# Kernel tuning notes

Measured on AMD Instinct MI355X. Metric: run time of the kernel, lower is better.

## Reference

```python
import jax, jax.numpy as jnp
import numpy as np

B, T, X_DIM = 8192, 100, 256
Y_DIM = 6
KSIZE = 50


def setup_inputs() -> dict:
    key = jax.random.key(0)
    k1, k2, k3 = jax.random.split(key, 3)
    sequence = jax.random.normal(k1, (B, T, X_DIM), dtype=jnp.float32)
    # per-feature Conv1d(1,1,k=50,bias=False) weights, stacked as depthwise kernel [X_DIM, 1, K]
    conv_w = jax.random.normal(k2, (X_DIM, 1, KSIZE), dtype=jnp.float32) * 0.1
    # Linear(x_dim -> y_dim*50, bias=False), torch layout [out, in]
    fc_w = jax.random.normal(k3, (Y_DIM * 50, X_DIM), dtype=jnp.float32) * 0.05
    return {"sequence": sequence, "conv_w": conv_w, "fc_w": fc_w}


def reference(sequence, conv_w, fc_w):
    # slice time window 30:100 and move features to channel dim: [B, X_DIM, 70]
    x = jnp.transpose(sequence[:, 30:100, :], (0, 2, 1))
    f = x.shape[1]
    # the Python loop of per-feature Conv1d(1,1,k) ops == one depthwise (grouped) conv
    y = jax.lax.conv_general_dilated(
        x, conv_w,
        window_strides=(1,), padding="VALID",
        dimension_numbers=("NCH", "OIH", "NCH"),
        feature_group_count=f,
    )  # [B, X_DIM, 21]
    # ReLU then max over time -> [B, X_DIM] (kernel_num == 1, so concat == this)
    feat = jnp.max(jax.nn.relu(y), axis=2)
    out = feat @ fc_w.T  # [B, Y_DIM*50]
    return out.reshape(-1, 50, Y_DIM)
```

## Files before the change

kernel.cpp:

```cpp
#include <hip/hip_runtime.h>

#define B_TOTAL 8192
#define T_FULL  100
#define XD      256
#define T0      30
#define TW      70
#define KS      50
#define NT      21
#define YOUT    300
#define FC_NB   16


#define DECLG(G) float G##0,G##1,G##2,G##3,G##4,G##5,G##6,G##7,G##8,G##9;

#define VMF(N) asm volatile("s_waitcnt vmcnt(" #N ")" ::: "memory")

#define GLL1(c, s, r) \
  __builtin_amdgcn_global_load_lds( \
      (const __attribute__((address_space(1))) void*)(xp + ((c)*10 + (r)) * XD), \
      (__attribute__((address_space(3))) void*)(ldsr + (s)*640 + (r)*64), 4, 0, 0);

#define GLL(c, s) \
  GLL1(c,s,0) GLL1(c,s,1) GLL1(c,s,2) GLL1(c,s,3) GLL1(c,s,4) \
  GLL1(c,s,5) GLL1(c,s,6) GLL1(c,s,7) GLL1(c,s,8) GLL1(c,s,9)

#define LOADL(G, s) \
  G##0=ldsr[(s)*640+  0+lane]; G##1=ldsr[(s)*640+ 64+lane]; \
  G##2=ldsr[(s)*640+128+lane]; G##3=ldsr[(s)*640+192+lane]; \
  G##4=ldsr[(s)*640+256+lane]; G##5=ldsr[(s)*640+320+lane]; \
  G##6=ldsr[(s)*640+384+lane]; G##7=ldsr[(s)*640+448+lane]; \
  G##8=ldsr[(s)*640+512+lane]; G##9=ldsr[(s)*640+576+lane];

#define LOADWSET(W, K0) \
  W##0=wtp[(K0+0)*XD]; W##1=wtp[(K0+1)*XD]; W##2=wtp[(K0+2)*XD]; W##3=wtp[(K0+3)*XD]; W##4=wtp[(K0+4)*XD]; \
  W##5=wtp[(K0+5)*XD]; W##6=wtp[(K0+6)*XD]; W##7=wtp[(K0+7)*XD]; W##8=wtp[(K0+8)*XD]; W##9=wtp[(K0+9)*XD];

#define ROW(A, W, X0,X1,X2,X3,X4,X5,X6,X7,X8,X9) \
  A=fmaf(X0,W##0,A); A=fmaf(X1,W##1,A); A=fmaf(X2,W##2,A); A=fmaf(X3,W##3,A); A=fmaf(X4,W##4,A); \
  A=fmaf(X5,W##5,A); A=fmaf(X6,W##6,A); A=fmaf(X7,W##7,A); A=fmaf(X8,W##8,A); A=fmaf(X9,W##9,A);

#define KB30(W, y0,y1,y2,y3,y4,y5,y6,y7,y8,y9,y10,y11,y12,y13,y14,y15,y16,y17,y18,y19,y20,y21,y22,y23,y24,y25,y26,y27,y28,y29) \
  ROW(a0 , W, y0 ,y1 ,y2 ,y3 ,y4 ,y5 ,y6 ,y7 ,y8 ,y9 ) \
  ROW(a1 , W, y1 ,y2 ,y3 ,y4 ,y5 ,y6 ,y7 ,y8 ,y9 ,y10) \
  ROW(a2 , W, y2 ,y3 ,y4 ,y5 ,y6 ,y7 ,y8 ,y9 ,y10,y11) \
  ROW(a3 , W, y3 ,y4 ,y5 ,y6 ,y7 ,y8 ,y9 ,y10,y11,y12) \
  ROW(a4 , W, y4 ,y5 ,y6 ,y7 ,y8 ,y9 ,y10,y11,y12,y13) \
  ROW(a5 , W, y5 ,y6 ,y7 ,y8 ,y9 ,y10,y11,y12,y13,y14) \
  ROW(a6 , W, y6 ,y7 ,y8 ,y9 ,y10,y11,y12,y13,y14,y15) \
  ROW(a7 , W, y7 ,y8 ,y9 ,y10,y11,y12,y13,y14,y15,y16) \
  ROW(a8 , W, y8 ,y9 ,y10,y11,y12,y13,y14,y15,y16,y17) \
  ROW(a9 , W, y9 ,y10,y11,y12,y13,y14,y15,y16,y17,y18) \
  ROW(a10, W, y10,y11,y12,y13,y14,y15,y16,y17,y18,y19) \
  ROW(a11, W, y11,y12,y13,y14,y15,y16,y17,y18,y19,y20) \
  ROW(a12, W, y12,y13,y14,y15,y16,y17,y18,y19,y20,y21) \
  ROW(a13, W, y13,y14,y15,y16,y17,y18,y19,y20,y21,y22) \
  ROW(a14, W, y14,y15,y16,y17,y18,y19,y20,y21,y22,y23) \
  ROW(a15, W, y15,y16,y17,y18,y19,y20,y21,y22,y23,y24) \
  ROW(a16, W, y16,y17,y18,y19,y20,y21,y22,y23,y24,y25) \
  ROW(a17, W, y17,y18,y19,y20,y21,y22,y23,y24,y25,y26) \
  ROW(a18, W, y18,y19,y20,y21,y22,y23,y24,y25,y26,y27) \
  ROW(a19, W, y19,y20,y21,y22,y23,y24,y25,y26,y27,y28) \
  ROW(a20, W, y20,y21,y22,y23,y24,y25,y26,y27,y28,y29)

#define KB30X(...) KB30(__VA_ARGS__)

#define GA xa0,xa1,xa2,xa3,xa4,xa5,xa6,xa7,xa8,xa9
#define GB xb0,xb1,xb2,xb3,xb4,xb5,xb6,xb7,xb8,xb9
#define GC xc0,xc1,xc2,xc3,xc4,xc5,xc6,xc7,xc8,xc9
#define GD xd0,xd1,xd2,xd3,xd4,xd5,xd6,xd7,xd8,xd9

__global__ __launch_bounds__(256)
void transpose_w(const float* __restrict__ conv_w, const float* __restrict__ fc_w,
                 float* __restrict__ wt, float* __restrict__ fct) {
    const int i = blockIdx.x * 256 + threadIdx.x;
    if (i < XD * KS) {
        const int f = i / KS;
        const int k = i - f * KS;
        wt[k * XD + f] = conv_w[i];
    }
    if (i < YOUT * XD) {
        const int o = i >> 8;
        const int q = i & 255;
        fct[q * YOUT + o] = fc_w[i];
    }
}

__global__ __launch_bounds__(256, 4)
void conv_kernel(const float* __restrict__ seq, const float* __restrict__ wt,
                 float* __restrict__ feat) {
    __shared__ float lds[4 * 4 * 640];
    const int lane = threadIdx.x & 63;
    const int wv   = threadIdx.x >> 6;
    const int b    = blockIdx.x;
    const float* xp  = seq + ((size_t)b * T_FULL + T0) * XD + threadIdx.x;
    const float* wtp = wt + threadIdx.x;
    float* ldsr = &lds[wv * 2560];

    float a0=0,a1=0,a2=0,a3=0,a4=0,a5=0,a6=0,a7=0,a8=0,a9=0,a10=0,
          a11=0,a12=0,a13=0,a14=0,a15=0,a16=0,a17=0,a18=0,a19=0,a20=0;
    DECLG(xa) DECLG(xb) DECLG(xc) DECLG(xd)
    DECLG(wa) DECLG(wb)

    GLL(0,0) GLL(1,1) GLL(2,2) GLL(3,3)
    LOADWSET(wa, 0); LOADWSET(wb, 10);
    VMF(50);  LOADL(xa, 0)
    VMF(40);  LOADL(xb, 1)
    GLL(4,0)
    VMF(30);  LOADL(xc, 2)
    KB30X(wa, GA, GB, GC)
    LOADWSET(wa, 20);
    GLL(5,1)
    VMF(50);  LOADL(xd, 3)
    KB30X(wb, GB, GC, GD)
    LOADWSET(wb, 30);
    GLL(6,2)
    VMF(40);  LOADL(xa, 0)
    KB30X(wa, GC, GD, GA)
    LOADWSET(wa, 40);
    VMF(30);  LOADL(xb, 1)
    KB30X(wb, GD, GA, GB)
    VMF(10);  LOADL(xc, 2)
    KB30X(wa, GA, GB, GC)

    float m = 0.f;
    m=fmaxf(m,a0 ); m=fmaxf(m,a1 ); m=fmaxf(m,a2 ); m=fmaxf(m,a3 ); m=fmaxf(m,a4 );
    m=fmaxf(m,a5 ); m=fmaxf(m,a6 ); m=fmaxf(m,a7 ); m=fmaxf(m,a8 ); m=fmaxf(m,a9 );
    m=fmaxf(m,a10); m=fmaxf(m,a11); m=fmaxf(m,a12); m=fmaxf(m,a13); m=fmaxf(m,a14);
    m=fmaxf(m,a15); m=fmaxf(m,a16); m=fmaxf(m,a17); m=fmaxf(m,a18); m=fmaxf(m,a19);
    m=fmaxf(m,a20);
    feat[(size_t)b * XD + threadIdx.x] = m;
}

#define FCSTEP(C, NB_) C = fmaf(wv_, fb[(NB_) * XD + q], C);

__global__ __launch_bounds__(320, 2)
void fc_kernel(const float* __restrict__ feat, const float* __restrict__ fct,
               float* __restrict__ out) {
    const int o  = threadIdx.x;
    const int b0 = blockIdx.x * FC_NB;
    if (o >= YOUT) return;

    const float* fb = feat + (size_t)b0 * XD;

    float c0=0,c1=0,c2=0,c3=0,c4=0,c5=0,c6=0,c7=0,
          c8=0,c9=0,c10=0,c11=0,c12=0,c13=0,c14=0,c15=0;

#pragma unroll 2
    for (int q = 0; q < XD; ++q) {
        const float wv_ = fct[q * YOUT + o];
        FCSTEP(c0 , 0)  FCSTEP(c1 , 1)  FCSTEP(c2 , 2)  FCSTEP(c3 , 3)
        FCSTEP(c4 , 4)  FCSTEP(c5 , 5)  FCSTEP(c6 , 6)  FCSTEP(c7 , 7)
        FCSTEP(c8 , 8)  FCSTEP(c9 , 9)  FCSTEP(c10,10)  FCSTEP(c11,11)
        FCSTEP(c12,12)  FCSTEP(c13,13)  FCSTEP(c14,14)  FCSTEP(c15,15)
    }

    out[(size_t)(b0 +  0) * YOUT + o] = c0;
    out[(size_t)(b0 +  1) * YOUT + o] = c1;
    out[(size_t)(b0 +  2) * YOUT + o] = c2;
    out[(size_t)(b0 +  3) * YOUT + o] = c3;
    out[(size_t)(b0 +  4) * YOUT + o] = c4;
    out[(size_t)(b0 +  5) * YOUT + o] = c5;
    out[(size_t)(b0 +  6) * YOUT + o] = c6;
    out[(size_t)(b0 +  7) * YOUT + o] = c7;
    out[(size_t)(b0 +  8) * YOUT + o] = c8;
    out[(size_t)(b0 +  9) * YOUT + o] = c9;
    out[(size_t)(b0 + 10) * YOUT + o] = c10;
    out[(size_t)(b0 + 11) * YOUT + o] = c11;
    out[(size_t)(b0 + 12) * YOUT + o] = c12;
    out[(size_t)(b0 + 13) * YOUT + o] = c13;
    out[(size_t)(b0 + 14) * YOUT + o] = c14;
    out[(size_t)(b0 + 15) * YOUT + o] = c15;
}

extern "C" void kernel_launch(void* const* d_in, const int* in_sizes, int n_in,
                              void* d_out, int out_size, void* d_ws, size_t ws_size,
                              hipStream_t stream) {
    const float* seq    = (const float*)d_in[0];
    const float* conv_w = (const float*)d_in[1];
    const float* fc_w   = (const float*)d_in[2];
    float*       out    = (float*)d_out;

    float* wt   = (float*)d_ws;
    float* fct  = wt  + XD * KS;
    float* feat = fct + XD * YOUT;

    transpose_w<<<dim3((YOUT * XD + 255) / 256), dim3(256), 0, stream>>>(conv_w, fc_w, wt, fct);
    conv_kernel<<<dim3(B_TOTAL), dim3(256), 0, stream>>>(seq, wt, feat);
    fc_kernel<<<dim3(B_TOTAL / FC_NB), dim3(320), 0, stream>>>(feat, fct, out);
}
```

Baseline: 184.9 us.

## Stage whole conv input window into LDS with 16-byte async loads

The conv kernel now loads the full 70x256 input window for a batch row into dynamic LDS up front. Each wave issues 16-byte global_load_lds per row instead of the earlier per-wave 4-byte streamed ring buffer with manual vmcnt waits, then synchronizes once and computes from LDS. This cuts the number of load instructions and the manual pipelining, but it no longer overlaps loading with compute inside a block. LDS use rises to 70 KB per block, and occupancy hint drops to 2 blocks per CU, with a third weight register set added.

```diff
diff --git a/kernel.cpp b/kernel.cpp
--- a/kernel.cpp
+++ b/kernel.cpp
@@ -13,23 +13,11 @@
 
 #define DECLG(G) float G##0,G##1,G##2,G##3,G##4,G##5,G##6,G##7,G##8,G##9;
 
-#define VMF(N) asm volatile("s_waitcnt vmcnt(" #N ")" ::: "memory")
-
-#define GLL1(c, s, r) \
-  __builtin_amdgcn_global_load_lds( \
-      (const __attribute__((address_space(1))) void*)(xp + ((c)*10 + (r)) * XD), \
-      (__attribute__((address_space(3))) void*)(ldsr + (s)*640 + (r)*64), 4, 0, 0);
-
-#define GLL(c, s) \
-  GLL1(c,s,0) GLL1(c,s,1) GLL1(c,s,2) GLL1(c,s,3) GLL1(c,s,4) \
-  GLL1(c,s,5) GLL1(c,s,6) GLL1(c,s,7) GLL1(c,s,8) GLL1(c,s,9)
-
-#define LOADL(G, s) \
-  G##0=ldsr[(s)*640+  0+lane]; G##1=ldsr[(s)*640+ 64+lane]; \
-  G##2=ldsr[(s)*640+128+lane]; G##3=ldsr[(s)*640+192+lane]; \
-  G##4=ldsr[(s)*640+256+lane]; G##5=ldsr[(s)*640+320+lane]; \
-  G##6=ldsr[(s)*640+384+lane]; G##7=ldsr[(s)*640+448+lane]; \
-  G##8=ldsr[(s)*640+512+lane]; G##9=ldsr[(s)*640+576+lane];
+#define LOADL(G, R0) \
+  G##0=ldsx[(R0+0)*XD+tid]; G##1=ldsx[(R0+1)*XD+tid]; G##2=ldsx[(R0+2)*XD+tid]; \
+  G##3=ldsx[(R0+3)*XD+tid]; G##4=ldsx[(R0+4)*XD+tid]; G##5=ldsx[(R0+5)*XD+tid]; \
+  G##6=ldsx[(R0+6)*XD+tid]; G##7=ldsx[(R0+7)*XD+tid]; G##8=ldsx[(R0+8)*XD+tid]; \
+  G##9=ldsx[(R0+9)*XD+tid];
 
 #define LOADWSET(W, K0) \
   W##0=wtp[(K0+0)*XD]; W##1=wtp[(K0+1)*XD]; W##2=wtp[(K0+2)*XD]; W##3=wtp[(K0+3)*XD]; W##4=wtp[(K0+4)*XD]; \
@@ -85,42 +73,49 @@
     }
 }
 
-__global__ __launch_bounds__(256, 4)
+__global__ __launch_bounds__(256, 2)
 void conv_kernel(const float* __restrict__ seq, const float* __restrict__ wt,
                  float* __restrict__ feat) {
-    __shared__ float lds[4 * 4 * 640];
-    const int lane = threadIdx.x & 63;
-    const int wv   = threadIdx.x >> 6;
+    extern __shared__ float ldsx[];
+    const int tid  = threadIdx.x;
+    const int lane = tid & 63;
+    const int wv   = tid >> 6;
     const int b    = blockIdx.x;
-    const float* xp  = seq + ((size_t)b * T_FULL + T0) * XD + threadIdx.x;
-    const float* wtp = wt + threadIdx.x;
-    float* ldsr = &lds[wv * 2560];
+    const float* wtp = wt + tid;
+
+    DECLG(wa) DECLG(wb) DECLG(wc)
+    LOADWSET(wa, 0); LOADWSET(wb, 10);
+
+    {
+        const float* rowbase = seq + ((size_t)b * T_FULL + T0) * XD + lane * 4;
+        const int r0 = wv * 18;
+        const int rn = (TW - r0 < 18) ? (TW - r0) : 18;
+        for (int i = 0; i < rn; ++i) {
+            __builtin_amdgcn_global_load_lds(
+                (const __attribute__((address_space(1))) void*)(rowbase + (size_t)(r0 + i) * XD),
+                (__attribute__((address_space(3))) void*)(ldsx + (r0 + i) * XD),
+                16, 0, 0);
+        }
+    }
+    __syncthreads();
 
     float a0=0,a1=0,a2=0,a3=0,a4=0,a5=0,a6=0,a7=0,a8=0,a9=0,a10=0,
           a11=0,a12=0,a13=0,a14=0,a15=0,a16=0,a17=0,a18=0,a19=0,a20=0;
     DECLG(xa) DECLG(xb) DECLG(xc) DECLG(xd)
-    DECLG(wa) DECLG(wb)
 
-    GLL(0,0) GLL(1,1) GLL(2,2) GLL(3,3)
-    LOADWSET(wa, 0); LOADWSET(wb, 10);
-    VMF(50);  LOADL(xa, 0)
-    VMF(40);  LOADL(xb, 1)
-    GLL(4,0)
-    VMF(30);  LOADL(xc, 2)
+    LOADL(xa, 0) LOADL(xb, 10) LOADL(xc, 20)
     KB30X(wa, GA, GB, GC)
-    LOADWSET(wa, 20);
-    GLL(5,1)
-    VMF(50);  LOADL(xd, 3)
+    LOADWSET(wc, 20);
+    LOADL(xd, 30)
     KB30X(wb, GB, GC, GD)
-    LOADWSET(wb, 30);
-    GLL(6,2)
-    VMF(40);  LOADL(xa, 0)
-    KB30X(wa, GC, GD, GA)
-    LOADWSET(wa, 40);
-    VMF(30);  LOADL(xb, 1)
-    KB30X(wb, GD, GA, GB)
-    VMF(10);  LOADL(xc, 2)
-    KB30X(wa, GA, GB, GC)
+    LOADWSET(wa, 30);
+    LOADL(xa, 40)
+    KB30X(wc, GC, GD, GA)
+    LOADWSET(wb, 40);
+    LOADL(xb, 50)
+    KB30X(wa, GD, GA, GB)
+    LOADL(xc, 60)
+    KB30X(wb, GA, GB, GC)
 
     float m = 0.f;
     m=fmaxf(m,a0 ); m=fmaxf(m,a1 ); m=fmaxf(m,a2 ); m=fmaxf(m,a3 ); m=fmaxf(m,a4 );
@@ -128,7 +123,7 @@
     m=fmaxf(m,a10); m=fmaxf(m,a11); m=fmaxf(m,a12); m=fmaxf(m,a13); m=fmaxf(m,a14);
     m=fmaxf(m,a15); m=fmaxf(m,a16); m=fmaxf(m,a17); m=fmaxf(m,a18); m=fmaxf(m,a19);
     m=fmaxf(m,a20);
-    feat[(size_t)b * XD + threadIdx.x] = m;
+    feat[(size_t)b * XD + tid] = m;
 }
 
 #define FCSTEP(C, NB_) C = fmaf(wv_, fb[(NB_) * XD + q], C);
@@ -185,6 +180,6 @@
     float* feat = fct + XD * YOUT;
 
     transpose_w<<<dim3((YOUT * XD + 255) / 256), dim3(256), 0, stream>>>(conv_w, fc_w, wt, fct);
-    conv_kernel<<<dim3(B_TOTAL), dim3(256), 0, stream>>>(seq, wt, feat);
+    conv_kernel<<<dim3(B_TOTAL), dim3(256), TW * XD * (int)sizeof(float), stream>>>(seq, wt, feat);
     fc_kernel<<<dim3(B_TOTAL / FC_NB), dim3(320), 0, stream>>>(feat, fct, out);
 }
```

After: 188.0 us. No clear change (+1.7%).
